# Optimization experiments

Hardware: AMD Instinct MI355X
Metric: run time of the kernel (lower is better)

The kernel has to match this reference:

```python
import jax, jax.numpy as jnp
import numpy as np

B, T1 = 256, 64            # batch, number of transition steps (T-1)
S, A = 128, 32             # state_size, action_size
BEL, HID, EMB = 1024, 1024, 1024
MIN_STD = 0.1


def _lin(key, out_dim, in_dim):
    k1, k2 = jax.random.split(key)
    s = 1.0 / np.sqrt(in_dim)
    W = jax.random.uniform(k1, (out_dim, in_dim), jnp.float32, -s, s)
    b = jax.random.uniform(k2, (out_dim,), jnp.float32, -s, s)
    return W, b


def setup_inputs() -> dict:
    key = jax.random.key(0)
    ks = jax.random.split(key, 16)
    W_sa, b_sa = _lin(ks[0], BEL, S + A)
    # GRUCell weights (torch layout: [3H, in]/[3H, H], gate order r,z,n)
    sg = 1.0 / np.sqrt(BEL)
    W_ih = jax.random.uniform(ks[1], (3 * BEL, BEL), jnp.float32, -sg, sg)
    W_hh = jax.random.uniform(ks[2], (3 * BEL, BEL), jnp.float32, -sg, sg)
    b_ih = jax.random.uniform(ks[3], (3 * BEL,), jnp.float32, -sg, sg)
    b_hh = jax.random.uniform(ks[4], (3 * BEL,), jnp.float32, -sg, sg)
    W_bp, b_bp = _lin(ks[5], HID, BEL)
    W_sp, b_sp = _lin(ks[6], 2 * S, HID)
    W_bq, b_bq = _lin(ks[7], HID, BEL + EMB)
    W_sq, b_sq = _lin(ks[8], 2 * S, HID)
    return {
        "prev_state": jax.random.normal(ks[9], (B, S), jnp.float32),
        "actions": jax.random.normal(ks[10], (T1, B, A), jnp.float32),
        "prev_belief": jax.random.normal(ks[11], (B, BEL), jnp.float32),
        "observations": jax.random.normal(ks[12], (T1, B, EMB), jnp.float32),
        "nonterminals": jnp.ones((T1, B, 1), jnp.float32),
        "prior_noise": jax.random.normal(ks[13], (T1, B, S), jnp.float32),
        "post_noise": jax.random.normal(ks[14], (T1, B, S), jnp.float32),
        "W_sa": W_sa, "b_sa": b_sa,
        "W_ih": W_ih, "W_hh": W_hh, "b_ih": b_ih, "b_hh": b_hh,
        "W_bp": W_bp, "b_bp": b_bp, "W_sp": W_sp, "b_sp": b_sp,
        "W_bq": W_bq, "b_bq": b_bq, "W_sq": W_sq, "b_sq": b_sq,
    }


def reference(prev_state, actions, prev_belief, observations, nonterminals,
              prior_noise, post_noise,
              W_sa, b_sa, W_ih, W_hh, b_ih, b_hh,
              W_bp, b_bp, W_sp, b_sp, W_bq, b_bq, W_sq, b_sq):
    # nonterminals[t-1] is applied for t>=1; t==0 uses no mask -> prepend ones
    nt_eff = jnp.concatenate([jnp.ones_like(nonterminals[:1]), nonterminals[:-1]], axis=0)

    def step(carry, inp):
        belief, state = carry
        a, obs, nt, pn, qn = inp
        s = state * nt
        x = jax.nn.relu(jnp.concatenate([s, a], axis=-1) @ W_sa.T + b_sa)
        h = belief * nt
        # torch GRUCell: gates r,z,n
        gi = x @ W_ih.T + b_ih
        gh = h @ W_hh.T + b_hh
        ir, iz, in_ = jnp.split(gi, 3, axis=-1)
        hr, hz, hn = jnp.split(gh, 3, axis=-1)
        r = jax.nn.sigmoid(ir + hr)
        z = jax.nn.sigmoid(iz + hz)
        n = jnp.tanh(in_ + r * hn)
        nb = (1.0 - z) * n + z * h  # new belief [B, BEL]
        # prior head
        hp = jax.nn.relu(nb @ W_bp.T + b_bp)
        pm, psd_raw = jnp.split(hp @ W_sp.T + b_sp, 2, axis=-1)
        psd = jax.nn.softplus(psd_raw) + MIN_STD
        ps = pm + psd * pn
        # posterior head
        hq = jax.nn.relu(jnp.concatenate([nb, obs], axis=-1) @ W_bq.T + b_bq)
        qm, qsd_raw = jnp.split(hq @ W_sq.T + b_sq, 2, axis=-1)
        qsd = jax.nn.softplus(qsd_raw) + MIN_STD
        qs = qm + qsd * qn
        return (nb, qs), (nb, ps, pm, psd, qs, qm, qsd)

    _, outs = jax.lax.scan(step, (prev_belief, prev_state),
                           (actions, observations, nt_eff, prior_noise, post_noise))
    beliefs, prior_states, prior_means, prior_stds, post_states, post_means, post_stds = outs
    return beliefs, prior_states, prior_means, prior_stds, post_states, post_means, post_stds
```

## Files before the change

### kernel.cpp

```cpp
#include <hip/hip_runtime.h>
#include <math.h>

constexpr int NB = 256, NT = 64, DS = 128, DA = 32, DB = 1024, DH = 1024, DE = 1024;
constexpr float MIN_STD = 0.1f;

constexpr size_t OUT_PS  = (size_t)NT * NB * DB;
constexpr size_t OUT_PM  = OUT_PS  + (size_t)NT * NB * DS;
constexpr size_t OUT_PSD = OUT_PM  + (size_t)NT * NB * DS;
constexpr size_t OUT_QS  = OUT_PSD + (size_t)NT * NB * DS;
constexpr size_t OUT_QM  = OUT_QS  + (size_t)NT * NB * DS;
constexpr size_t OUT_QSD = OUT_QM  + (size_t)NT * NB * DS;

typedef __attribute__((ext_vector_type(8))) short bf8_t;
typedef __attribute__((ext_vector_type(4))) float f4_t;
#define MFMA16(a, b, c) __builtin_amdgcn_mfma_f32_16x16x32_bf16((a), (b), (c), 0, 0, 0)
#define SWZ8(ch, row) ((ch & ~7) | ((ch & 7) ^ ((row) & 7)))

__device__ __forceinline__ short f2bf(float f) {
    union { float f; unsigned u; } v; v.f = f;
    unsigned r = v.u + 0x7FFF + ((v.u >> 16) & 1);
    return (short)(r >> 16);
}
__device__ __forceinline__ float bf2f(unsigned short h) {
    union { unsigned u; float f; } v; v.u = ((unsigned)h) << 16; return v.f;
}
__device__ __forceinline__ unsigned pack2(float a, float b) {
    return ((unsigned)(unsigned short)f2bf(a)) | (((unsigned)(unsigned short)f2bf(b)) << 16);
}
__device__ __forceinline__ float sigm(float x) { return 1.0f / (1.0f + __expf(-x)); }

__global__ __launch_bounds__(256) void k_cvt_all(
    const float* __restrict__ Wih, const float* __restrict__ Whh,
    const float* __restrict__ Wbp, const float* __restrict__ Wbq,
    const float* __restrict__ Wsp, const float* __restrict__ Wsq,
    const float* __restrict__ Wsa,
    short* dWbp, short* dWbq, short* dWsp, short* dWsq,
    short* dWsqsw, short* dWsasw, short* dWbqnb, short* dWihsw, short* dWhhsw)
{
    int i = blockIdx.x * 256 + threadIdx.x;
    if (i >= 1429504) return;
    if (i >= 512000 && i < 643072) {
        int il = i - 512000;
        int c = il >> 7, kc = il & 127;
        const float4* s4 = (const float4*)Wbq;
        float4 a = s4[(size_t)c * 512 + kc * 2], b = s4[(size_t)c * 512 + kc * 2 + 1];
        bf8_t v;
        v[0]=f2bf(a.x); v[1]=f2bf(a.y); v[2]=f2bf(a.z); v[3]=f2bf(a.w);
        v[4]=f2bf(b.x); v[5]=f2bf(b.y); v[6]=f2bf(b.z); v[7]=f2bf(b.w);
        ((bf8_t*)dWbqnb)[((size_t)((c >> 4) * 128 + kc)) * 16 + (c & 15)] = v;
        return;
    }
    const float* src; short* dst; int lo; bool sw = false; int swNCH = 0;
    if      (i <  131072) { src = Wbp; dst = dWbp; lo = 0; }
    else if (i <  393216) { src = Wbq; dst = dWbq; lo = 131072; }
    else if (i <  425984) { src = Wsp; dst = dWsp; lo = 393216; }
    else if (i <  458752) { src = Wsq; dst = dWsq; lo = 425984; }
    else if (i <  491520) { src = Wsq; dst = dWsqsw; lo = 458752; sw = true; swNCH = 128; }
    else if (i <  512000) { src = Wsa; dst = dWsasw; lo = 491520; sw = true; swNCH = 20; }
    else if (i < 1036288) { src = Wih; dst = dWihsw; lo = 643072;  sw = true; swNCH = 128; }
    else                  { src = Whh; dst = dWhhsw; lo = 1036288; sw = true; swNCH = 128; }
    int il = i - lo;
    const float4* s4 = (const float4*)src;
    float4 a = s4[il * 2], b = s4[il * 2 + 1];
    bf8_t v;
    v[0]=f2bf(a.x); v[1]=f2bf(a.y); v[2]=f2bf(a.z); v[3]=f2bf(a.w);
    v[4]=f2bf(b.x); v[5]=f2bf(b.y); v[6]=f2bf(b.z); v[7]=f2bf(b.w);
    if (!sw) ((bf8_t*)dst)[il] = v;
    else {
        int row = il / swNCH, ch = il % swNCH;
        ((bf8_t*)dst)[((row >> 4) * swNCH + ch) * 16 + (row & 15)] = v;
    }
}

__global__ __launch_bounds__(256) void kobs(
    const float* __restrict__ obsA, const short* __restrict__ Wbq_bf,
    const float* __restrict__ b_bq, short* __restrict__ dst)
{
    __shared__ __align__(16) char smem[16384];
    const int tx = threadIdx.x;
    const int wv = tx >> 6, lane = tx & 63;
    const int b0 = blockIdx.y * 64, j0 = blockIdx.x * 64;
    const int wm = wv & 1, wn = wv >> 1;
    const bf8_t* Wq8 = (const bf8_t*)Wbq_bf;
    bf8_t* sA = (bf8_t*)smem;
    bf8_t* sB = sA + 512;
    f4_t acc[2][2];
    acc[0][0] = (f4_t)0.0f; acc[0][1] = (f4_t)0.0f;
    acc[1][0] = (f4_t)0.0f; acc[1][1] = (f4_t)0.0f;

    for (int kt = 0; kt < DE; kt += 64) {
        #pragma unroll
        for (int i = 0; i < 2; ++i) {
            int c = tx + i * 256;
            int row = c >> 3, ch = c & 7;
            const float4* p4 = (const float4*)(obsA + (size_t)(b0 + row) * DE + kt + ch * 8);
            float4 f0 = p4[0], f1 = p4[1];
            bf8_t v;
            v[0]=f2bf(f0.x); v[1]=f2bf(f0.y); v[2]=f2bf(f0.z); v[3]=f2bf(f0.w);
            v[4]=f2bf(f1.x); v[5]=f2bf(f1.y); v[6]=f2bf(f1.z); v[7]=f2bf(f1.w);
            sA[row * 8 + (ch ^ (row & 7))] = v;
            sB[row * 8 + (ch ^ (row & 7))] = Wq8[(size_t)(j0 + row) * 256 + 128 + (kt >> 3) + ch];
        }
        __syncthreads();
        #pragma unroll
        for (int ks = 0; ks < 2; ++ks) {
            int ch = ks * 4 + (lane >> 4);
            bf8_t a[2], b[2];
            #pragma unroll
            for (int mi = 0; mi < 2; ++mi) {
                int row = wm * 32 + mi * 16 + (lane & 15);
                a[mi] = sA[row * 8 + (ch ^ (row & 7))];
            }
            #pragma unroll
            for (int ni = 0; ni < 2; ++ni) {
                int row = wn * 32 + ni * 16 + (lane & 15);
                b[ni] = sB[row * 8 + (ch ^ (row & 7))];
            }
            #pragma unroll
            for (int mi = 0; mi < 2; ++mi)
                #pragma unroll
                for (int ni = 0; ni < 2; ++ni)
                    acc[mi][ni] = MFMA16(a[mi], b[ni], acc[mi][ni]);
        }
        __syncthreads();
    }
    float* ebuf = (float*)smem;
    #pragma unroll
    for (int mi = 0; mi < 2; ++mi)
        #pragma unroll
        for (int ni = 0; ni < 2; ++ni)
            #pragma unroll
            for (int r = 0; r < 4; ++r) {
                int row = wm * 32 + mi * 16 + (lane >> 4) * 4 + r;
                int col = wn * 32 + ni * 16 + (lane & 15);
                ebuf[row * 64 + col] = acc[mi][ni][r] + b_bq[j0 + col];
            }
    __syncthreads();
    {
        int bl = tx >> 2, p = tx & 3;
        float* src = ebuf + bl * 64 + p * 16;
        short* d = dst + (size_t)(b0 + bl) * DB + j0 + p * 16;
        #pragma unroll
        for (int q = 0; q < 4; ++q) {
            uint2 u; u.x = pack2(src[q*4], src[q*4+1]); u.y = pack2(src[q*4+2], src[q*4+3]);
            *(uint2*)(d + q * 4) = u;
        }
    }
}

__global__ __launch_bounds__(1024) void kstep(
    int t,
    const float* __restrict__ prev_state, const float* __restrict__ actions_t,
    const float* __restrict__ nonterm, const float* __restrict__ post_noise,
    const short* __restrict__ nbb_prev, const short* __restrict__ obs_pre_tm1,
    const short* __restrict__ Wsq_sw, const float* __restrict__ b_sq,
    const short* __restrict__ Wsa_sw, const float* __restrict__ b_sa,
    const short* __restrict__ Wih_sw, const short* __restrict__ Whh_sw,
    const float* __restrict__ b_ih, const float* __restrict__ b_hh,
    const short* __restrict__ Wbqnb_sw,
    const float* __restrict__ belp,
    float* __restrict__ bel_out, short* __restrict__ nbb_out,
    float* __restrict__ o_qm, float* __restrict__ o_qsd, float* __restrict__ o_qs)
{
    __shared__ __align__(16) char smem[124160];
    short* R1s = (short*)smem;
    bf8_t* R18 = (bf8_t*)smem;
    float* qex = (float*)smem;
    bf8_t* hf8 = (bf8_t*)(smem + 32768);
    short* saS = (short*)(smem + 65536);
    bf8_t* sa8 = (bf8_t*)(smem + 65536);
    bf8_t* nbS = (bf8_t*)(smem + 70912);
    float* exg = (float*)(smem + 70912);
    float* exn = (float*)(smem + 120064);

    const int tx = threadIdx.x, bid = blockIdx.x;
    const int wv = tx >> 6, lane = tx & 63;
    const int ar = lane & 15, kq = lane >> 4;
    const int bgrp = bid >> 4, low = bid & 15;
    const int jt = ((low & 7) << 1) | (low >> 3);
    const int b0 = bgrp * 16, j0 = jt * 64;
    const float* ntp = (t > 0) ? nonterm + (size_t)(t - 1) * NB : nullptr;

    if (t > 0) {
        #pragma unroll
        for (int i = 0; i < 2; ++i) {
            int c = tx + i * 1024;
            int row = c >> 7, ch = c & 127;
            nbS[row * 128 + SWZ8(ch, row)] =
                ((const bf8_t*)nbb_prev)[(size_t)(b0 + row) * 128 + ch];
        }
        __syncthreads();
        {
            f4_t hacc[4];
            #pragma unroll
            for (int i = 0; i < 4; ++i) hacc[i] = (f4_t)0.0f;
            for (int ks = 0; ks < 32; ++ks) {
                int ch = ks * 4 + kq;
                bf8_t a = nbS[ar * 128 + SWZ8(ch, ar)];
                #pragma unroll
                for (int i = 0; i < 4; ++i) {
                    int tile = wv * 4 + i;
                    bf8_t bfr = *(const bf8_t*)(Wbqnb_sw +
                        (((size_t)tile * 128 + ch) * 16 + ar) * 8);
                    hacc[i] = MFMA16(a, bfr, hacc[i]);
                }
            }
            #pragma unroll
            for (int i = 0; i < 4; ++i) {
                int col = (wv * 4 + i) * 16 + ar;
                int chunk = col >> 3, el = col & 7;
                #pragma unroll
                for (int r = 0; r < 4; ++r) {
                    int row = kq * 4 + r;
                    float z = hacc[i][r] +
                        bf2f((unsigned short)obs_pre_tm1[(size_t)(b0 + row) * DB + col]);
                    R1s[row * 1024 + SWZ8(chunk, row) * 8 + el] = f2bf(fmaxf(z, 0.0f));
                }
            }
        }
        __syncthreads();
        {
            f4_t qa[4];
            #pragma unroll
            for (int i = 0; i < 4; ++i) qa[i] = (f4_t)0.0f;
            for (int ks = 0; ks < 32; ks += 4) {
                #pragma unroll
                for (int u = 0; u < 4; ++u) {
                    int ch = (ks + u) * 4 + kq;
                    bf8_t a = R18[ar * 128 + SWZ8(ch, ar)];
                    bf8_t bfr = *(const bf8_t*)(Wsq_sw +
                        ((size_t)(wv * 128 + ch)) * 128 + ar * 8);
                    qa[u] = MFMA16(a, bfr, qa[u]);
                }
            }
            f4_t qs_ = (qa[0] + qa[1]) + (qa[2] + qa[3]);
            __syncthreads();
            #pragma unroll
            for (int r = 0; r < 4; ++r)
                qex[(kq * 4 + r) * 257 + wv * 16 + ar] = qs_[r];
        }
        __syncthreads();
        #pragma unroll
        for (int i = 0; i < 2; ++i) {
            int e = tx + i * 1024;
            int row = e >> 7, col = e & 127;
            int b = b0 + row;
            float m  = qex[row * 257 + col] + b_sq[col];
            float sr = qex[row * 257 + 128 + col] + b_sq[128 + col];
            float sd = log1pf(__expf(-fabsf(sr))) + fmaxf(sr, 0.0f) + MIN_STD;
            float n_ = post_noise[((size_t)(t - 1) * NB + b) * DS + col];
            float qs = fmaf(sd, n_, m);
            if (jt == 0) {
                size_t off = ((size_t)(t - 1) * NB + b) * DS + col;
                o_qm[off] = m; o_qsd[off] = sd; o_qs[off] = qs;
            }
            saS[row * 168 + col] = f2bf(qs * ntp[b]);
        }
    } else {
        #pragma unroll
        for (int i = 0; i < 2; ++i) {
            int e = tx + i * 1024;
            int row = e >> 7, col = e & 127;
            saS[row * 168 + col] = f2bf(prev_state[(size_t)(b0 + row) * DS + col]);
        }
    }
    if (tx < 512) {
        int row = tx >> 5, ac = tx & 31;
        saS[row * 168 + 128 + ac] = f2bf(actions_t[(size_t)(b0 + row) * DA + ac]);
    }
    __syncthreads();

    {
        f4_t xacc[4];
        #pragma unroll
        for (int i = 0; i < 4; ++i) xacc[i] = (f4_t)0.0f;
        #pragma unroll
        for (int ks = 0; ks < 5; ++ks) {
            int ch = ks * 4 + kq;
            bf8_t a = sa8[ar * 21 + ch];
            #pragma unroll
            for (int i = 0; i < 4; ++i) {
                int tile = wv * 4 + i;
                bf8_t bfr = *(const bf8_t*)(Wsa_sw +
                    ((size_t)(tile * 20 + ch)) * 128 + ar * 8);
                xacc[i] = MFMA16(a, bfr, xacc[i]);
            }
        }
        #pragma unroll
        for (int i = 0; i < 4; ++i) {
            int col = (wv * 4 + i) * 16 + ar;
            float bj = b_sa[col];
            int chunk = col >> 3, el = col & 7;
            #pragma unroll
            for (int r = 0; r < 4; ++r) {
                int row = kq * 4 + r;
                R1s[row * 1024 + SWZ8(chunk, row) * 8 + el] =
                    f2bf(fmaxf(xacc[i][r] + bj, 0.0f));
            }
        }
    }
    #pragma unroll
    for (int i = 0; i < 2; ++i) {
        int c = tx + i * 1024;
        int row = c >> 7, ch = c & 127;
        int b = b0 + row;
        const float4* p4 = (const float4*)(belp + (size_t)b * DB + ch * 8);
        float4 f0 = p4[0], f1 = p4[1];
        float ntv = ntp ? ntp[b] : 1.0f;
        bf8_t v;
        v[0]=f2bf(f0.x*ntv); v[1]=f2bf(f0.y*ntv); v[2]=f2bf(f0.z*ntv); v[3]=f2bf(f0.w*ntv);
        v[4]=f2bf(f1.x*ntv); v[5]=f2bf(f1.y*ntv); v[6]=f2bf(f1.z*ntv); v[7]=f2bf(f1.w*ntv);
        hf8[row * 128 + SWZ8(ch, row)] = v;
    }
    __syncthreads();

    {
        const int kh = wv >> 3, wg = (wv >> 2) & 1, wn = wv & 3;
        f4_t acc[3];
        acc[0] = (f4_t)0.0f; acc[1] = (f4_t)0.0f; acc[2] = (f4_t)0.0f;
        const bf8_t* Asrc = wg ? hf8 : R18;
        const short* Wsw = wg ? Whh_sw : Wih_sw;
        #pragma unroll 4
        for (int k16 = 0; k16 < 16; ++k16) {
            int chunk = kh * 64 + k16 * 4 + kq;
            bf8_t a = Asrc[ar * 128 + SWZ8(chunk, ar)];
            #pragma unroll
            for (int g = 0; g < 3; ++g) {
                bf8_t bfr = *(const bf8_t*)(Wsw +
                    (((size_t)(g * 64 + jt * 4 + wn) * 128 + chunk) * 16 + ar) * 8);
                acc[g] = MFMA16(a, bfr, acc[g]);
            }
        }
        #pragma unroll
        for (int g = 0; g < 3; ++g)
            #pragma unroll
            for (int r = 0; r < 4; ++r)
                exg[((wv * 3 + g) * 16 + (kq * 4 + r)) * 16 + ar] = acc[g][r];
    }
    __syncthreads();
    if (wv < 4) {
        const int wn2 = wv, cl = ar;
        const int j = j0 + wn2 * 16 + cl;
        const float bir = b_ih[j], biz = b_ih[DB + j], bin = b_ih[2 * DB + j];
        const float bhr = b_hh[j], bhz = b_hh[DB + j], bhn = b_hh[2 * DB + j];
        #pragma unroll
        for (int r = 0; r < 4; ++r) {
            const int row = kq * 4 + r;
            const int b = b0 + row;
            float gi[3], gh[3];
            #pragma unroll
            for (int g = 0; g < 3; ++g) {
                gi[g] = exg[(((0  + wn2) * 3 + g) * 16 + row) * 16 + cl]
                      + exg[(((8  + wn2) * 3 + g) * 16 + row) * 16 + cl];
                gh[g] = exg[(((4  + wn2) * 3 + g) * 16 + row) * 16 + cl]
                      + exg[(((12 + wn2) * 3 + g) * 16 + row) * 16 + cl];
            }
            const float ntv = ntp ? ntp[b] : 1.0f;
            const float h = belp[(size_t)b * DB + j] * ntv;
            const float rr = sigm(gi[0] + bir + gh[0] + bhr);
            const float zz = sigm(gi[1] + biz + gh[1] + bhz);
            const float nn = tanhf(gi[2] + bin + rr * (gh[2] + bhn));
            exn[row * 64 + wn2 * 16 + cl] = (1.0f - zz) * nn + zz * h;
        }
    }
    __syncthreads();
    {
        int row = tx >> 6, col = tx & 63;
        bel_out[(size_t)(b0 + row) * DB + j0 + col] = exn[row * 64 + col];
    }
    if (tx < 512) {
        int row = tx >> 5, cp = tx & 31;
        unsigned pv = pack2(exn[row * 64 + cp * 2], exn[row * 64 + cp * 2 + 1]);
        *(unsigned*)(nbb_out + (size_t)(b0 + row) * DB + j0 + cp * 2) = pv;
    }
}

__global__ __launch_bounds__(256) void khq(
    const short* __restrict__ nbb, const float* __restrict__ obs_t,
    const short* __restrict__ Wbq_bf, const float* __restrict__ b_bq,
    short* __restrict__ hqb)
{
    __shared__ __align__(16) char smem[12288];
    const int q = blockIdx.x, tx = threadIdx.x;
    const int wv = tx >> 6, lane = tx & 63;
    const int b0 = (q >> 5) * 64, j0 = (q & 31) * 32;
    const int wm = wv & 1, wn = wv >> 1;
    const bf8_t* nb8 = (const bf8_t*)nbb;
    const bf8_t* Wq8 = (const bf8_t*)Wbq_bf;
    bf8_t* sA = (bf8_t*)smem;
    bf8_t* sB = sA + 512;
    f4_t acc[2];
    acc[0] = (f4_t)0.0f; acc[1] = (f4_t)0.0f;

    for (int kt = 0; kt < DB + DE; kt += 64) {
        #pragma unroll
        for (int i = 0; i < 2; ++i) {
            int c = tx + i * 256;
            int row = c >> 3, ch = c & 7, b = b0 + row;
            bf8_t v;
            if (kt < DB) {
                v = nb8[(size_t)b * 128 + (kt >> 3) + ch];
            } else {
                const float4* p4 = (const float4*)(obs_t + (size_t)b * DE + (kt - DB) + ch * 8);
                float4 f0 = p4[0], f1 = p4[1];
                v[0]=f2bf(f0.x); v[1]=f2bf(f0.y); v[2]=f2bf(f0.z); v[3]=f2bf(f0.w);
                v[4]=f2bf(f1.x); v[5]=f2bf(f1.y); v[6]=f2bf(f1.z); v[7]=f2bf(f1.w);
            }
            sA[row * 8 + (ch ^ (row & 7))] = v;
        }
        {
            int row = tx >> 3, ch = tx & 7;
            sB[row * 8 + (ch ^ (row & 7))] = Wq8[(size_t)(j0 + row) * 256 + (kt >> 3) + ch];
        }
        __syncthreads();
        #pragma unroll
        for (int ks = 0; ks < 2; ++ks) {
            int ch = ks * 4 + (lane >> 4);
            bf8_t a[2], b;
            #pragma unroll
            for (int mi = 0; mi < 2; ++mi) {
                int row = wm * 32 + mi * 16 + (lane & 15);
                a[mi] = sA[row * 8 + (ch ^ (row & 7))];
            }
            {
                int row = wn * 16 + (lane & 15);
                b = sB[row * 8 + (ch ^ (row & 7))];
            }
            acc[0] = MFMA16(a[0], b, acc[0]);
            acc[1] = MFMA16(a[1], b, acc[1]);
        }
        __syncthreads();
    }
    float* ebuf = (float*)smem;
    #pragma unroll
    for (int mi = 0; mi < 2; ++mi)
        #pragma unroll
        for (int r = 0; r < 4; ++r) {
            int row = wm * 32 + mi * 16 + (lane >> 4) * 4 + r;
            int col = wn * 16 + (lane & 15);
            ebuf[row * 32 + col] = fmaxf(acc[mi][r] + b_bq[j0 + col], 0.0f);
        }
    __syncthreads();
    {
        int bl = tx >> 2, p = tx & 3;
        float* src = ebuf + bl * 32 + p * 8;
        short* dst = hqb + (size_t)(b0 + bl) * DH + j0 + p * 8;
        #pragma unroll
        for (int q2 = 0; q2 < 2; ++q2) {
            uint2 u; u.x = pack2(src[q2*4], src[q2*4+1]); u.y = pack2(src[q2*4+2], src[q2*4+3]);
            *(uint2*)(dst + q2 * 4) = u;
        }
    }
}

__global__ __launch_bounds__(256) void kout(
    const short* __restrict__ A_, const short* __restrict__ W_,
    const float* __restrict__ bias, const float* __restrict__ noise,
    float* __restrict__ om, float* __restrict__ osd, float* __restrict__ os)
{
    __shared__ __align__(16) char smem[12288];
    const int tx = threadIdx.x;
    const int wv = tx >> 6, lane = tx & 63;
    const int b0 = blockIdx.y * 64, i0 = blockIdx.x * 16;
    const int wm = wv & 1, wn = wv >> 1;
    const bf8_t* A8 = (const bf8_t*)A_;
    const bf8_t* W8 = (const bf8_t*)W_;
    bf8_t* sA = (bf8_t*)smem;
    bf8_t* sB = sA + 512;
    f4_t acc[2];
    acc[0] = (f4_t)0.0f; acc[1] = (f4_t)0.0f;

    for (int kt = 0; kt < DH; kt += 64) {
        #pragma unroll
        for (int i = 0; i < 2; ++i) {
            int c = tx + i * 256;
            int row = c >> 3, ch = c & 7;
            sA[row * 8 + (ch ^ (row & 7))] = A8[(size_t)(b0 + row) * 128 + (kt >> 3) + ch];
        }
        {
            int row = tx >> 3, ch = tx & 7;
            int wr = (row < 16) ? (i0 + row) : (128 + i0 + (row - 16));
            sB[row * 8 + (ch ^ (row & 7))] = W8[(size_t)wr * 128 + (kt >> 3) + ch];
        }
        __syncthreads();
        #pragma unroll
        for (int ks = 0; ks < 2; ++ks) {
            int ch = ks * 4 + (lane >> 4);
            bf8_t a[2], b;
            #pragma unroll
            for (int mi = 0; mi < 2; ++mi) {
                int row = wm * 32 + mi * 16 + (lane & 15);
                a[mi] = sA[row * 8 + (ch ^ (row & 7))];
            }
            {
                int row = wn * 16 + (lane & 15);
                b = sB[row * 8 + (ch ^ (row & 7))];
            }
            acc[0] = MFMA16(a[0], b, acc[0]);
            acc[1] = MFMA16(a[1], b, acc[1]);
        }
        __syncthreads();
    }
    float* ebuf = (float*)smem;
    #pragma unroll
    for (int mi = 0; mi < 2; ++mi)
        #pragma unroll
        for (int r = 0; r < 4; ++r) {
            int row = wm * 32 + mi * 16 + (lane >> 4) * 4 + r;
            int col = wn * 16 + (lane & 15);
            ebuf[row * 32 + col] = acc[mi][r];
        }
    __syncthreads();
    {
        int bl = tx >> 2, p = tx & 3;
        int b = b0 + bl;
        float4 vm, vs, vx;
        #pragma unroll
        for (int k = 0; k < 4; ++k) {
            int i = p * 4 + k;
            float m_ = ebuf[bl * 32 + i] + bias[i0 + i];
            float sraw = ebuf[bl * 32 + 16 + i] + bias[128 + i0 + i];
            float sd = log1pf(__expf(-fabsf(sraw))) + fmaxf(sraw, 0.0f) + MIN_STD;
            float n_ = noise[(size_t)b * DS + i0 + i];
            ((float*)&vm)[k] = m_;
            ((float*)&vs)[k] = sd;
            ((float*)&vx)[k] = fmaf(sd, n_, m_);
        }
        size_t off = (size_t)b * DS + i0 + p * 4;
        *(float4*)(om + off)  = vm;
        *(float4*)(osd + off) = vs;
        *(float4*)(os + off)  = vx;
    }
}

__global__ __launch_bounds__(256) void khp(
    const float* __restrict__ belA, const short* __restrict__ Wbp_bf,
    const float* __restrict__ b_bp, short* __restrict__ hp_bf)
{
    __shared__ __align__(16) char smem[16384];
    const int tx = threadIdx.x;
    const int wv = tx >> 6, lane = tx & 63;
    const int b0 = blockIdx.y * 64, j0 = blockIdx.x * 64;
    const int wm = wv & 1, wn = wv >> 1;
    const bf8_t* Wp8 = (const bf8_t*)Wbp_bf;
    bf8_t* sA = (bf8_t*)smem;
    bf8_t* sB = sA + 512;
    f4_t acc[2][2];
    acc[0][0] = (f4_t)0.0f; acc[0][1] = (f4_t)0.0f;
    acc[1][0] = (f4_t)0.0f; acc[1][1] = (f4_t)0.0f;

    for (int kt = 0; kt < DB; kt += 64) {
        #pragma unroll
        for (int i = 0; i < 2; ++i) {
            int c = tx + i * 256;
            int row = c >> 3, ch = c & 7;
            const float4* p4 = (const float4*)(belA + (size_t)(b0 + row) * DB + kt + ch * 8);
            float4 f0 = p4[0], f1 = p4[1];
            bf8_t v;
            v[0]=f2bf(f0.x); v[1]=f2bf(f0.y); v[2]=f2bf(f0.z); v[3]=f2bf(f0.w);
            v[4]=f2bf(f1.x); v[5]=f2bf(f1.y); v[6]=f2bf(f1.z); v[7]=f2bf(f1.w);
            sA[row * 8 + (ch ^ (row & 7))] = v;
            sB[row * 8 + (ch ^ (row & 7))] = Wp8[(size_t)(j0 + row) * 128 + (kt >> 3) + ch];
        }
        __syncthreads();
        #pragma unroll
        for (int ks = 0; ks < 2; ++ks) {
            int ch = ks * 4 + (lane >> 4);
            bf8_t a[2], b[2];
            #pragma unroll
            for (int mi = 0; mi < 2; ++mi) {
                int row = wm * 32 + mi * 16 + (lane & 15);
                a[mi] = sA[row * 8 + (ch ^ (row & 7))];
            }
            #pragma unroll
            for (int ni = 0; ni < 2; ++ni) {
                int row = wn * 32 + ni * 16 + (lane & 15);
                b[ni] = sB[row * 8 + (ch ^ (row & 7))];
            }
            #pragma unroll
            for (int mi = 0; mi < 2; ++mi)
                #pragma unroll
                for (int ni = 0; ni < 2; ++ni)
                    acc[mi][ni] = MFMA16(a[mi], b[ni], acc[mi][ni]);
        }
        __syncthreads();
    }
    float* ebuf = (float*)smem;
    #pragma unroll
    for (int mi = 0; mi < 2; ++mi)
        #pragma unroll
        for (int ni = 0; ni < 2; ++ni)
            #pragma unroll
            for (int r = 0; r < 4; ++r) {
                int row = wm * 32 + mi * 16 + (lane >> 4) * 4 + r;
                int col = wn * 32 + ni * 16 + (lane & 15);
                ebuf[row * 64 + col] = fmaxf(acc[mi][ni][r] + b_bp[j0 + col], 0.0f);
            }
    __syncthreads();
    {
        int bl = tx >> 2, p = tx & 3;
        float* src = ebuf + bl * 64 + p * 16;
        short* dst = hp_bf + (size_t)(b0 + bl) * DH + j0 + p * 16;
        #pragma unroll
        for (int q = 0; q < 4; ++q) {
            uint2 u; u.x = pack2(src[q*4], src[q*4+1]); u.y = pack2(src[q*4+2], src[q*4+3]);
            *(uint2*)(dst + q * 4) = u;
        }
    }
}

extern "C" void kernel_launch(void* const* d_in, const int* in_sizes, int n_in,
                              void* d_out, int out_size, void* d_ws, size_t ws_size,
                              hipStream_t stream)
{
    const float* prev_state   = (const float*)d_in[0];
    const float* actions      = (const float*)d_in[1];
    const float* prev_belief  = (const float*)d_in[2];
    const float* observations = (const float*)d_in[3];
    const float* nonterm      = (const float*)d_in[4];
    const float* prior_noise  = (const float*)d_in[5];
    const float* post_noise   = (const float*)d_in[6];
    const float* W_sa = (const float*)d_in[7];
    const float* b_sa = (const float*)d_in[8];
    const float* W_ih = (const float*)d_in[9];
    const float* W_hh = (const float*)d_in[10];
    const float* b_ih = (const float*)d_in[11];
    const float* b_hh = (const float*)d_in[12];
    const float* W_bp = (const float*)d_in[13];
    const float* b_bp = (const float*)d_in[14];
    const float* W_sp = (const float*)d_in[15];
    const float* b_sp = (const float*)d_in[16];
    const float* W_bq = (const float*)d_in[17];
    const float* b_bq = (const float*)d_in[18];
    const float* W_sq = (const float*)d_in[19];
    const float* b_sq = (const float*)d_in[20];

    float* out     = (float*)d_out;
    float* beliefs = out;
    float* o_ps  = out + OUT_PS;
    float* o_pm  = out + OUT_PM;
    float* o_psd = out + OUT_PSD;
    float* o_qs  = out + OUT_QS;
    float* o_qm  = out + OUT_QM;
    float* o_qsd = out + OUT_QSD;

    short* w = (short*)d_ws;
    short* Wbp_bf   = w;
    short* Wbq_bf   = Wbp_bf   + (size_t)1048576;
    short* Wsp_bf   = Wbq_bf   + (size_t)2097152;
    short* Wsq_bf   = Wsp_bf   + (size_t)262144;
    short* Wsq_sw   = Wsq_bf   + (size_t)262144;
    short* Wsa_sw   = Wsq_sw   + (size_t)262144;
    short* Wbqnb_sw = Wsa_sw   + (size_t)163840;
    short* Wih_sw   = Wbqnb_sw + (size_t)1048576;
    short* Whh_sw   = Wih_sw   + (size_t)3145728;
    short* obs_ch   = Whh_sw   + (size_t)3145728;
    short* nbb      = obs_ch   + (size_t)4194304;
    short* hqb      = nbb      + (size_t)524288;
    short* hp_bf    = hqb      + (size_t)262144;
    const size_t NBB = (size_t)NB * DB;

    k_cvt_all<<<5584, 256, 0, stream>>>(
        W_ih, W_hh, W_bp, W_bq, W_sp, W_sq, W_sa,
        Wbp_bf, Wbq_bf, Wsp_bf, Wsq_bf, Wsq_sw, Wsa_sw, Wbqnb_sw, Wih_sw, Whh_sw);

    for (int t = 0; t < NT; ++t) {
        const float* belp = (t == 0) ? prev_belief : beliefs + (size_t)(t - 1) * NB * DB;
        kstep<<<256, 1024, 0, stream>>>(
            t, prev_state, actions + (size_t)t * NB * DA,
            nonterm, post_noise,
            nbb + ((t & 1) ^ 1) * NBB,
            obs_ch + (size_t)((t + 15) & 15) * NB * DB,
            Wsq_sw, b_sq, Wsa_sw, b_sa,
            Wih_sw, Whh_sw, b_ih, b_hh, Wbqnb_sw,
            belp, beliefs + (size_t)t * NB * DB,
            nbb + (t & 1) * NBB,
            o_qm, o_qsd, o_qs);
        if ((t & 15) == 0)
            kobs<<<dim3(16, 64), 256, 0, stream>>>(
                observations + (size_t)t * NB * DE, Wbq_bf, b_bq, obs_ch);
    }

    khq<<<128, 256, 0, stream>>>(
        nbb + ((NT - 1) & 1) * NBB, observations + (size_t)(NT - 1) * NB * DE,
        Wbq_bf, b_bq, hqb);
    kout<<<dim3(8, 4), 256, 0, stream>>>(
        hqb, Wsq_bf, b_sq, post_noise + (size_t)(NT - 1) * NB * DS,
        o_qm + (size_t)(NT - 1) * NB * DS, o_qsd + (size_t)(NT - 1) * NB * DS,
        o_qs + (size_t)(NT - 1) * NB * DS);

    for (int c = 0; c < 4; ++c) {
        const size_t r0 = (size_t)c * 4096;
        khp<<<dim3(16, 64), 256, 0, stream>>>(
            beliefs + r0 * DB, Wbp_bf, b_bp, hp_bf);
        kout<<<dim3(8, 64), 256, 0, stream>>>(
            hp_bf, Wsp_bf, b_sp, prior_noise + r0 * DS,
            o_pm + r0 * DS, o_psd + r0 * DS, o_ps + r0 * DS);
    }
}
```

Measured before the change: 3.187 ms.

## Split posterior-hidden GEMM into per-block partial products reduced next step

Instead of each kstep block loading the full previous bf16 belief and running a full K=1024 GEMM against the belief half of W_bq, each block now computes a K=64 partial product from its own freshly computed belief slice and writes it to a 16-way partials buffer. The next step sums the 16 partials plus the precomputed observation term and applies ReLU, which replaces the redundant per-block GEMM with a cheap reduction. The final-step hidden computation likewise becomes a simple partial-sum kernel. The trade-off is much more global memory traffic for the bf16 partials, and summing rounded bf16 partials adds extra precision loss.

```diff
diff --git a/kernel.cpp b/kernel.cpp
--- a/kernel.cpp
+++ b/kernel.cpp
@@ -152,14 +152,14 @@
     int t,
     const float* __restrict__ prev_state, const float* __restrict__ actions_t,
     const float* __restrict__ nonterm, const float* __restrict__ post_noise,
-    const short* __restrict__ nbb_prev, const short* __restrict__ obs_pre_tm1,
+    const short* __restrict__ part_in, const short* __restrict__ obs_pre_tm1,
     const short* __restrict__ Wsq_sw, const float* __restrict__ b_sq,
     const short* __restrict__ Wsa_sw, const float* __restrict__ b_sa,
     const short* __restrict__ Wih_sw, const short* __restrict__ Whh_sw,
     const float* __restrict__ b_ih, const float* __restrict__ b_hh,
     const short* __restrict__ Wbqnb_sw,
     const float* __restrict__ belp,
-    float* __restrict__ bel_out, short* __restrict__ nbb_out,
+    float* __restrict__ bel_out, short* __restrict__ part_out,
     float* __restrict__ o_qm, float* __restrict__ o_qsd, float* __restrict__ o_qs)
 {
     __shared__ __align__(16) char smem[124160];
@@ -167,9 +167,9 @@
     bf8_t* R18 = (bf8_t*)smem;
     float* qex = (float*)smem;
     bf8_t* hf8 = (bf8_t*)(smem + 32768);
+    bf8_t* sP  = (bf8_t*)(smem + 32768);
     short* saS = (short*)(smem + 65536);
     bf8_t* sa8 = (bf8_t*)(smem + 65536);
-    bf8_t* nbS = (bf8_t*)(smem + 70912);
     float* exg = (float*)(smem + 70912);
     float* exn = (float*)(smem + 120064);
 
@@ -186,37 +186,20 @@
         for (int i = 0; i < 2; ++i) {
             int c = tx + i * 1024;
             int row = c >> 7, ch = c & 127;
-            nbS[row * 128 + SWZ8(ch, row)] =
-                ((const bf8_t*)nbb_prev)[(size_t)(b0 + row) * 128 + ch];
-        }
-        __syncthreads();
-        {
-            f4_t hacc[4];
-            #pragma unroll
-            for (int i = 0; i < 4; ++i) hacc[i] = (f4_t)0.0f;
-            for (int ks = 0; ks < 32; ++ks) {
-                int ch = ks * 4 + kq;
-                bf8_t a = nbS[ar * 128 + SWZ8(ch, ar)];
+            const bf8_t o8 = ((const bf8_t*)obs_pre_tm1)[(size_t)(b0 + row) * 128 + ch];
+            float s[8];
+            #pragma unroll
+            for (int e = 0; e < 8; ++e) s[e] = bf2f((unsigned short)o8[e]);
+            #pragma unroll
+            for (int p = 0; p < 16; ++p) {
+                const bf8_t v = ((const bf8_t*)part_in)[((size_t)p * NB + b0 + row) * 128 + ch];
                 #pragma unroll
-                for (int i = 0; i < 4; ++i) {
-                    int tile = wv * 4 + i;
-                    bf8_t bfr = *(const bf8_t*)(Wbqnb_sw +
-                        (((size_t)tile * 128 + ch) * 16 + ar) * 8);
-                    hacc[i] = MFMA16(a, bfr, hacc[i]);
-                }
-            }
-            #pragma unroll
-            for (int i = 0; i < 4; ++i) {
-                int col = (wv * 4 + i) * 16 + ar;
-                int chunk = col >> 3, el = col & 7;
-                #pragma unroll
-                for (int r = 0; r < 4; ++r) {
-                    int row = kq * 4 + r;
-                    float z = hacc[i][r] +
-                        bf2f((unsigned short)obs_pre_tm1[(size_t)(b0 + row) * DB + col]);
-                    R1s[row * 1024 + SWZ8(chunk, row) * 8 + el] = f2bf(fmaxf(z, 0.0f));
-                }
-            }
+                for (int e = 0; e < 8; ++e) s[e] += bf2f((unsigned short)v[e]);
+            }
+            bf8_t r;
+            #pragma unroll
+            for (int e = 0; e < 8; ++e) r[e] = f2bf(fmaxf(s[e], 0.0f));
+            R18[row * 128 + SWZ8(ch, row)] = r;
         }
         __syncthreads();
         {
@@ -368,89 +351,57 @@
         int row = tx >> 6, col = tx & 63;
         bel_out[(size_t)(b0 + row) * DB + j0 + col] = exn[row * 64 + col];
     }
-    if (tx < 512) {
-        int row = tx >> 5, cp = tx & 31;
-        unsigned pv = pack2(exn[row * 64 + cp * 2], exn[row * 64 + cp * 2 + 1]);
-        *(unsigned*)(nbb_out + (size_t)(b0 + row) * DB + j0 + cp * 2) = pv;
-    }
-}
-
-__global__ __launch_bounds__(256) void khq(
-    const short* __restrict__ nbb, const float* __restrict__ obs_t,
-    const short* __restrict__ Wbq_bf, const float* __restrict__ b_bq,
+    if (tx < 128) {
+        int row = tx >> 3, ch = tx & 7;
+        const float* s = exn + row * 64 + ch * 8;
+        bf8_t v;
+        v[0]=f2bf(s[0]); v[1]=f2bf(s[1]); v[2]=f2bf(s[2]); v[3]=f2bf(s[3]);
+        v[4]=f2bf(s[4]); v[5]=f2bf(s[5]); v[6]=f2bf(s[6]); v[7]=f2bf(s[7]);
+        sP[row * 8 + (ch ^ (row & 7))] = v;
+    }
+    __syncthreads();
+    {
+        f4_t pacc[4];
+        #pragma unroll
+        for (int i = 0; i < 4; ++i) pacc[i] = (f4_t)0.0f;
+        #pragma unroll
+        for (int ks = 0; ks < 2; ++ks) {
+            int ch = ks * 4 + kq;
+            bf8_t a = sP[ar * 8 + (ch ^ (ar & 7))];
+            #pragma unroll
+            for (int i = 0; i < 4; ++i) {
+                int tile = wv * 4 + i;
+                bf8_t bfr = *(const bf8_t*)(Wbqnb_sw +
+                    (((size_t)tile * 128 + jt * 8 + ch) * 16 + ar) * 8);
+                pacc[i] = MFMA16(a, bfr, pacc[i]);
+            }
+        }
+        #pragma unroll
+        for (int i = 0; i < 4; ++i) {
+            int c = (wv * 4 + i) * 16 + ar;
+            #pragma unroll
+            for (int r = 0; r < 4; ++r)
+                part_out[((size_t)jt * NB + b0 + kq * 4 + r) * DB + c] = f2bf(pacc[i][r]);
+        }
+    }
+}
+
+__global__ __launch_bounds__(256) void khq63(
+    const short* __restrict__ partials, const short* __restrict__ obs_pre,
     short* __restrict__ hqb)
 {
-    __shared__ __align__(16) char smem[12288];
-    const int q = blockIdx.x, tx = threadIdx.x;
-    const int wv = tx >> 6, lane = tx & 63;
-    const int b0 = (q >> 5) * 64, j0 = (q & 31) * 32;
-    const int wm = wv & 1, wn = wv >> 1;
-    const bf8_t* nb8 = (const bf8_t*)nbb;
-    const bf8_t* Wq8 = (const bf8_t*)Wbq_bf;
-    bf8_t* sA = (bf8_t*)smem;
-    bf8_t* sB = sA + 512;
-    f4_t acc[2];
-    acc[0] = (f4_t)0.0f; acc[1] = (f4_t)0.0f;
-
-    for (int kt = 0; kt < DB + DE; kt += 64) {
-        #pragma unroll
-        for (int i = 0; i < 2; ++i) {
-            int c = tx + i * 256;
-            int row = c >> 3, ch = c & 7, b = b0 + row;
-            bf8_t v;
-            if (kt < DB) {
-                v = nb8[(size_t)b * 128 + (kt >> 3) + ch];
-            } else {
-                const float4* p4 = (const float4*)(obs_t + (size_t)b * DE + (kt - DB) + ch * 8);
-                float4 f0 = p4[0], f1 = p4[1];
-                v[0]=f2bf(f0.x); v[1]=f2bf(f0.y); v[2]=f2bf(f0.z); v[3]=f2bf(f0.w);
-                v[4]=f2bf(f1.x); v[5]=f2bf(f1.y); v[6]=f2bf(f1.z); v[7]=f2bf(f1.w);
-            }
-            sA[row * 8 + (ch ^ (row & 7))] = v;
-        }
-        {
-            int row = tx >> 3, ch = tx & 7;
-            sB[row * 8 + (ch ^ (row & 7))] = Wq8[(size_t)(j0 + row) * 256 + (kt >> 3) + ch];
-        }
-        __syncthreads();
-        #pragma unroll
-        for (int ks = 0; ks < 2; ++ks) {
-            int ch = ks * 4 + (lane >> 4);
-            bf8_t a[2], b;
-            #pragma unroll
-            for (int mi = 0; mi < 2; ++mi) {
-                int row = wm * 32 + mi * 16 + (lane & 15);
-                a[mi] = sA[row * 8 + (ch ^ (row & 7))];
-            }
-            {
-                int row = wn * 16 + (lane & 15);
-                b = sB[row * 8 + (ch ^ (row & 7))];
-            }
-            acc[0] = MFMA16(a[0], b, acc[0]);
-            acc[1] = MFMA16(a[1], b, acc[1]);
-        }
-        __syncthreads();
-    }
-    float* ebuf = (float*)smem;
-    #pragma unroll
-    for (int mi = 0; mi < 2; ++mi)
-        #pragma unroll
-        for (int r = 0; r < 4; ++r) {
-            int row = wm * 32 + mi * 16 + (lane >> 4) * 4 + r;
-            int col = wn * 16 + (lane & 15);
-            ebuf[row * 32 + col] = fmaxf(acc[mi][r] + b_bq[j0 + col], 0.0f);
-        }
-    __syncthreads();
-    {
-        int bl = tx >> 2, p = tx & 3;
-        float* src = ebuf + bl * 32 + p * 8;
-        short* dst = hqb + (size_t)(b0 + bl) * DH + j0 + p * 8;
-        #pragma unroll
-        for (int q2 = 0; q2 < 2; ++q2) {
-            uint2 u; u.x = pack2(src[q2*4], src[q2*4+1]); u.y = pack2(src[q2*4+2], src[q2*4+3]);
-            *(uint2*)(dst + q2 * 4) = u;
-        }
-    }
+    const int row = blockIdx.x;
+    const int c = threadIdx.x * 4;
+    const ushort4 o = *(const ushort4*)(obs_pre + (size_t)row * DB + c);
+    float s0 = bf2f(o.x), s1 = bf2f(o.y), s2 = bf2f(o.z), s3 = bf2f(o.w);
+    for (int p = 0; p < 16; ++p) {
+        const ushort4 v = *(const ushort4*)(partials + ((size_t)p * NB + row) * DB + c);
+        s0 += bf2f(v.x); s1 += bf2f(v.y); s2 += bf2f(v.z); s3 += bf2f(v.w);
+    }
+    uint2 u;
+    u.x = pack2(fmaxf(s0, 0.0f), fmaxf(s1, 0.0f));
+    u.y = pack2(fmaxf(s2, 0.0f), fmaxf(s3, 0.0f));
+    *(uint2*)(hqb + (size_t)row * DB + c) = u;
 }
 
 __global__ __launch_bounds__(256) void kout(
@@ -655,10 +606,10 @@
     short* Wih_sw   = Wbqnb_sw + (size_t)1048576;
     short* Whh_sw   = Wih_sw   + (size_t)3145728;
     short* obs_ch   = Whh_sw   + (size_t)3145728;
-    short* nbb      = obs_ch   + (size_t)4194304;
-    short* hqb      = nbb      + (size_t)524288;
+    short* partials = obs_ch   + (size_t)4194304;
+    short* hqb      = partials + (size_t)8388608;
     short* hp_bf    = hqb      + (size_t)262144;
-    const size_t NBB = (size_t)NB * DB;
+    const size_t PART = (size_t)16 * NB * DB;
 
     k_cvt_all<<<5584, 256, 0, stream>>>(
         W_ih, W_hh, W_bp, W_bq, W_sp, W_sq, W_sa,
@@ -669,21 +620,20 @@
         kstep<<<256, 1024, 0, stream>>>(
             t, prev_state, actions + (size_t)t * NB * DA,
             nonterm, post_noise,
-            nbb + ((t & 1) ^ 1) * NBB,
+            partials + ((t & 1) ^ 1) * PART,
             obs_ch + (size_t)((t + 15) & 15) * NB * DB,
             Wsq_sw, b_sq, Wsa_sw, b_sa,
             Wih_sw, Whh_sw, b_ih, b_hh, Wbqnb_sw,
             belp, beliefs + (size_t)t * NB * DB,
-            nbb + (t & 1) * NBB,
+            partials + (t & 1) * PART,
             o_qm, o_qsd, o_qs);
         if ((t & 15) == 0)
             kobs<<<dim3(16, 64), 256, 0, stream>>>(
                 observations + (size_t)t * NB * DE, Wbq_bf, b_bq, obs_ch);
     }
 
-    khq<<<128, 256, 0, stream>>>(
-        nbb + ((NT - 1) & 1) * NBB, observations + (size_t)(NT - 1) * NB * DE,
-        Wbq_bf, b_bq, hqb);
+    khq63<<<256, 256, 0, stream>>>(
+        partials + ((NT - 1) & 1) * PART, obs_ch + (size_t)15 * NB * DB, hqb);
     kout<<<dim3(8, 4), 256, 0, stream>>>(
         hqb, Wsq_bf, b_sq, post_noise + (size_t)(NT - 1) * NB * DS,
         o_qm + (size_t)(NT - 1) * NB * DS, o_qsd + (size_t)(NT - 1) * NB * DS,
```

After: 2.723 ms. 14.6% less time.
